# Optimization experiments

Hardware: AMD Instinct MI355X
Metric: run time of the kernel (lower is better)

The kernel has to match this reference:

```python
import jax, jax.numpy as jnp
import numpy as np

# --- Cl(5,0) geometric algebra with 32 basis blades (bitmask representation) ---
def _cayley():
    def sgn(a, b):
        # sign from reordering basis vectors (Euclidean metric: no metric signs)
        a >>= 1
        s = 0
        while a:
            s += bin(a & b).count('1')
            a >>= 1
        return -1.0 if (s & 1) else 1.0
    C = np.zeros((32, 32, 32), np.float32)
    for i in range(32):
        for j in range(32):
            C[i, j, i ^ j] = sgn(i, j)
    return jnp.asarray(C)

CAYLEY = _cayley()  # [32,32,32] structure constants
EPS = 1e-8

def geometric_product(a, b):
    # a, b: [..., 32]
    return jnp.einsum('...i,...j,ijk->...k', a, b, CAYLEY)

def manifold_normalization(x):
    # project multivector back to the unit-norm manifold
    return x * jax.lax.rsqrt(jnp.sum(x * x, axis=-1, keepdims=True) + EPS)


def setup_inputs() -> dict:
    key = jax.random.key(0)
    k1, k2, k3 = jax.random.split(key, 3)
    B, S, N, D = 16, 256, 16, 6
    H = 16  # hidden_channels
    x = jax.random.normal(k1, (B, S, N, D), dtype=jnp.float32)
    W_in = jax.random.normal(k2, (D, H * 32), dtype=jnp.float32) * 0.1
    b_in = jnp.zeros((H * 32,), dtype=jnp.float32)
    W_out = jax.random.normal(k3, (H * 32, D), dtype=jnp.float32) * 0.05
    b_out = jnp.zeros((D,), dtype=jnp.float32)
    return {"x": x, "W_in": W_in, "b_in": b_in, "W_out": W_out, "b_out": b_out}


def reference(x, W_in, b_in, W_out, b_out):
    B, S, N, D = x.shape
    H = W_in.shape[1] // 32
    # proj_in over the whole sequence at once
    x_embs = (x @ W_in + b_in).reshape(B, S, N, H, 32)
    # psi init: identity rotor (scalar blade = 1)
    psi0 = jnp.zeros((B, N, H, 32), dtype=x.dtype).at[..., 0].set(1.0)

    def step(psi, inp):
        u_t, x_t = inp  # [B,N,H,32], [B,N,D]
        delta_r = manifold_normalization(u_t.at[..., 0].add(1.0))
        psi = manifold_normalization(geometric_product(delta_r, psi))
        pred_delta = psi.reshape(B, N, H * 32) @ W_out + b_out
        return psi, x_t + pred_delta

    _, ys = jax.lax.scan(step, psi0,
                         (jnp.swapaxes(x_embs, 0, 1), jnp.swapaxes(x, 0, 1)))
    return jnp.swapaxes(ys, 0, 1)  # [B,S,N,D]
```

## Files before the change

### kernel.cpp

```cpp
#include <hip/hip_runtime.h>


#define EPS 1e-8f

constexpr int pcnt(int v) { int s = 0; while (v) { s += v & 1; v >>= 1; } return s; }
constexpr float sgnf(int a, int b) {
    a >>= 1; int s = 0;
    while (a) { s += pcnt(a & b); a >>= 1; }
    return (s & 1) ? -1.0f : 1.0f;
}
struct Tab16 {
    float sg2[16][16];
    float sig[16];
    int   cm[16];
};
constexpr Tab16 make16() {
    Tab16 t{};
    for (int c = 0; c < 16; ++c) {
        int m = c | ((pcnt(c) & 1) << 4);
        t.cm[c] = m;
        t.sig[c] = sgnf(m ^ 31, 31);
    }
    for (int i = 0; i < 16; ++i)
        for (int j = 0; j < 16; ++j)
            t.sg2[i][j] = sgnf(t.cm[i], t.cm[j]);
    return t;
}
__device__ constexpr Tab16 T16 = make16();

__global__ __launch_bounds__(256, 1) void k_prep(
        const float* __restrict__ W_in, const float* __restrict__ b_in,
        float* __restrict__ WP) {
    const int idx = blockIdx.x * 256 + threadIdx.x;
    if (idx >= 16 * 224) return;
    const int h = idx / 224, r = idx % 224;
    const int sg = r / 112, r2 = r % 112;
    const float pm = sg ? -1.0f : 1.0f;
    float val;
    if (r2 < 96) {
        const int d = r2 >> 4, c = r2 & 15, m = T16.cm[c];
        val = W_in[d * 512 + h * 32 + m]
            + pm * T16.sig[c] * W_in[d * 512 + h * 32 + (m ^ 31)];
    } else {
        const int c = r2 - 96, m = T16.cm[c];
        val = b_in[h * 32 + m] + pm * T16.sig[c] * b_in[h * 32 + (m ^ 31)];
    }
    WP[idx] = val;
}

__device__ __forceinline__ void build_u16(const float* __restrict__ Wsp,
                                          const float xv[6], float U[16]) {
#pragma unroll
    for (int c = 0; c < 16; ++c) U[c] = Wsp[96 + c];
#pragma unroll
    for (int d = 0; d < 6; ++d)
#pragma unroll
        for (int c = 0; c < 16; ++c)
            U[c] = fmaf(xv[d], Wsp[d * 16 + c], U[c]);
    U[0] += 1.0f;
}

__device__ __forceinline__ void gp16(float* __restrict__ np,
                                     const float* __restrict__ U,
                                     const float* __restrict__ R) {
#pragma unroll
    for (int c1 = 0; c1 < 16; ++c1)
#pragma unroll
        for (int c2 = 0; c2 < 16; ++c2)
            np[c1 ^ c2] = fmaf(T16.sg2[c1][c2] * U[c1], R[c2], np[c1 ^ c2]);
}

__device__ __forceinline__ float ssum32(const float* a, const float* b) {
    float s0 = 0.f, s1 = 0.f, s2 = 0.f, s3 = 0.f;
#pragma unroll
    for (int k = 0; k < 16; k += 4) {
        s0 = fmaf(a[k],     a[k],     s0); s1 = fmaf(a[k + 1], a[k + 1], s1);
        s2 = fmaf(a[k + 2], a[k + 2], s2); s3 = fmaf(a[k + 3], a[k + 3], s3);
        s0 = fmaf(b[k],     b[k],     s0); s1 = fmaf(b[k + 1], b[k + 1], s1);
        s2 = fmaf(b[k + 2], b[k + 2], s2); s3 = fmaf(b[k + 3], b[k + 3], s3);
    }
    return (s0 + s1) + (s2 + s3);
}

__global__ __launch_bounds__(256, 1) void k_fused(
        const float* __restrict__ x, const float* __restrict__ WP,
        const float* __restrict__ W_out, float* __restrict__ WS2) {
    const int lane = threadIdx.x & 63;
    const int wid = __builtin_amdgcn_readfirstlane(
        (int)(blockIdx.x * 4 + (threadIdx.x >> 6)));
    const int h = wid & 15, p = wid >> 4;
    const int sc = lane & 31;
    const int bn = p * 2 + (lane >> 5), b = bn >> 4, n = bn & 15;
    const float* __restrict__ Wp0 = WP + h * 224;
    const float* __restrict__ Wp1 = WP + h * 224 + 112;
    const float* __restrict__ Oh  = W_out + h * 192;

    float Ap[16], Am[16];
    {
        const int t = sc * 8;
        const float2* xp = (const float2*)(x + ((b * 256 + t) * 16 + n) * 6);
        float2 x01 = xp[0], x23 = xp[1], x45 = xp[2];
        const float xv[6] = {x01.x, x01.y, x23.x, x23.y, x45.x, x45.y};
        build_u16(Wp0, xv, Ap);
        build_u16(Wp1, xv, Am);
    }
    for (int i = 1; i < 8; ++i) {
        const int t = sc * 8 + i;
        const float2* xp = (const float2*)(x + ((b * 256 + t) * 16 + n) * 6);
        float2 x01 = xp[0], x23 = xp[1], x45 = xp[2];
        const float xv[6] = {x01.x, x01.y, x23.x, x23.y, x45.x, x45.y};
        float U[16], np[16];
        build_u16(Wp0, xv, U);
#pragma unroll
        for (int k = 0; k < 16; ++k) np[k] = 0.0f;
        gp16(np, U, Ap);
#pragma unroll
        for (int k = 0; k < 16; ++k) Ap[k] = np[k];
        build_u16(Wp1, xv, U);
#pragma unroll
        for (int k = 0; k < 16; ++k) np[k] = 0.0f;
        gp16(np, U, Am);
#pragma unroll
        for (int k = 0; k < 16; ++k) Am[k] = np[k];
    }
    {
        float rs = rsqrtf(0.5f * ssum32(Ap, Am) + EPS);
#pragma unroll
        for (int k = 0; k < 16; ++k) { Ap[k] *= rs; Am[k] *= rs; }
    }

#pragma unroll
    for (int k = 1; k < 32; k <<= 1) {
        float prp[16], prm[16];
#pragma unroll
        for (int j = 0; j < 16; ++j) {
            prp[j] = __shfl_up(Ap[j], k, 32);
            prm[j] = __shfl_up(Am[j], k, 32);
        }
        if (sc >= k) {
            float np[16];
#pragma unroll
            for (int m = 0; m < 16; ++m) np[m] = 0.0f;
            gp16(np, Ap, prp);
#pragma unroll
            for (int m = 0; m < 16; ++m) Ap[m] = np[m];
#pragma unroll
            for (int m = 0; m < 16; ++m) np[m] = 0.0f;
            gp16(np, Am, prm);
#pragma unroll
            for (int m = 0; m < 16; ++m) Am[m] = np[m];
        }
    }
    {
        float rs = rsqrtf(0.5f * ssum32(Ap, Am) + EPS);
#pragma unroll
        for (int j = 0; j < 16; ++j) { Ap[j] *= rs; Am[j] *= rs; }
    }
    float Rp[16], Rm[16];
#pragma unroll
    for (int j = 0; j < 16; ++j) {
        Rp[j] = __shfl_up(Ap[j], 1, 32);
        Rm[j] = __shfl_up(Am[j], 1, 32);
    }
    if (sc == 0) {
#pragma unroll
        for (int j = 0; j < 16; ++j) { Rp[j] = 0.0f; Rm[j] = 0.0f; }
        Rp[0] = 1.0f; Rm[0] = 1.0f;
    }

    for (int i = 0; i < 8; ++i) {
        const int t = sc * 8 + i;
        const float2* xp = (const float2*)(x + ((b * 256 + t) * 16 + n) * 6);
        float2 x01 = xp[0], x23 = xp[1], x45 = xp[2];
        const float xv[6] = {x01.x, x01.y, x23.x, x23.y, x45.x, x45.y};
        float U[16], npp[16], npm[16];
        build_u16(Wp0, xv, U);
#pragma unroll
        for (int k = 0; k < 16; ++k) npp[k] = 0.0f;
        gp16(npp, U, Rp);
        build_u16(Wp1, xv, U);
#pragma unroll
        for (int k = 0; k < 16; ++k) npm[k] = 0.0f;
        gp16(npm, U, Rm);
        float rs = 0.5f * rsqrtf(0.5f * ssum32(npp, npm) + EPS);
        float pd[6] = {0.f, 0.f, 0.f, 0.f, 0.f, 0.f};
#pragma unroll
        for (int c = 0; c < 16; ++c) {
            const int m = T16.cm[c];
            const float ev = npp[c] + npm[c];
            const float od = T16.sig[c] * (npp[c] - npm[c]);
#pragma unroll
            for (int d = 0; d < 6; ++d) {
                pd[d] = fmaf(ev, Oh[m * 6 + d], pd[d]);
                pd[d] = fmaf(od, Oh[(m ^ 31) * 6 + d], pd[d]);
            }
        }
#pragma unroll
        for (int k = 0; k < 16; ++k) { Rp[k] = npp[k]; Rm[k] = npm[k]; }
        float2* wp = (float2*)(WS2 + (((t * 16 + h) * 256) + bn) * 6);
        wp[0] = make_float2(pd[0] * rs, pd[1] * rs);
        wp[1] = make_float2(pd[2] * rs, pd[3] * rs);
        wp[2] = make_float2(pd[4] * rs, pd[5] * rs);
    }
}

__global__ __launch_bounds__(256, 1) void k_reduce(
        const float* __restrict__ x, const float* __restrict__ b_out,
        const float* __restrict__ WS2, float* __restrict__ out) {
    const int o = blockIdx.x * 256 + threadIdx.x;
    const int d = o % 6;
    const int r = o / 6;
    const int n = r & 15;
    const int r2 = r >> 4;
    const int t = r2 & 255;
    const int b = r2 >> 8;
    const int bn = b * 16 + n;
    float acc = x[o] + b_out[d];
#pragma unroll
    for (int h = 0; h < 16; ++h)
        acc += WS2[(((t * 16 + h) * 256) + bn) * 6 + d];
    out[o] = acc;
}

extern "C" void kernel_launch(void* const* d_in, const int* in_sizes, int n_in,
                              void* d_out, int out_size, void* d_ws, size_t ws_size,
                              hipStream_t stream) {
    (void)in_sizes; (void)n_in; (void)out_size; (void)ws_size;
    const float* x     = (const float*)d_in[0];
    const float* W_in  = (const float*)d_in[1];
    const float* b_in  = (const float*)d_in[2];
    const float* W_out = (const float*)d_in[3];
    const float* b_out = (const float*)d_in[4];
    float* out = (float*)d_out;

    float* WP  = (float*)d_ws;
    float* WS2 = (float*)((char*)d_ws + 16384);

    k_prep  <<<14,   256, 0, stream>>>(W_in, b_in, WP);
    k_fused <<<512,  256, 0, stream>>>(x, WP, W_out, WS2);
    k_reduce<<<1536, 256, 0, stream>>>(x, b_out, WS2, out);
}
```

Before: 144.7 us.

## Fuse head reduction into scan kernel via shared memory, widen scan to 64 lanes

Each block now handles one (b,n) pair with 16 waves (one per head), each wave scanning 256 timesteps with 64 lanes of 4 steps each instead of 32 lanes of 8. Per-head output contributions go to LDS, and after a barrier the block sums the 16 heads and writes the output directly. This removes the separate reduce kernel and the global workspace round trip. The cost is a longer parallel prefix scan (6 levels instead of 5), 96KB of LDS per block, and only 256 blocks of 1024 threads.

```diff
diff --git a/kernel.cpp b/kernel.cpp
--- a/kernel.cpp
+++ b/kernel.cpp
@@ -82,30 +82,32 @@
     return (s0 + s1) + (s2 + s3);
 }
 
-__global__ __launch_bounds__(256, 1) void k_fused(
+__global__ __launch_bounds__(1024, 1) void k_fused(
         const float* __restrict__ x, const float* __restrict__ WP,
-        const float* __restrict__ W_out, float* __restrict__ WS2) {
-    const int lane = threadIdx.x & 63;
-    const int wid = __builtin_amdgcn_readfirstlane(
-        (int)(blockIdx.x * 4 + (threadIdx.x >> 6)));
-    const int h = wid & 15, p = wid >> 4;
-    const int sc = lane & 31;
-    const int bn = p * 2 + (lane >> 5), b = bn >> 4, n = bn & 15;
+        const float* __restrict__ W_out, const float* __restrict__ b_out,
+        float* __restrict__ out) {
+    __shared__ float LP[16 * 1536];
+
+    const int tid  = threadIdx.x;
+    const int lane = tid & 63;
+    const int h = __builtin_amdgcn_readfirstlane((int)(tid >> 6));
+    const int bn = blockIdx.x, b = bn >> 4, n = bn & 15;
+    const int sc = lane;
     const float* __restrict__ Wp0 = WP + h * 224;
     const float* __restrict__ Wp1 = WP + h * 224 + 112;
     const float* __restrict__ Oh  = W_out + h * 192;
 
     float Ap[16], Am[16];
     {
-        const int t = sc * 8;
+        const int t = sc * 4;
         const float2* xp = (const float2*)(x + ((b * 256 + t) * 16 + n) * 6);
         float2 x01 = xp[0], x23 = xp[1], x45 = xp[2];
         const float xv[6] = {x01.x, x01.y, x23.x, x23.y, x45.x, x45.y};
         build_u16(Wp0, xv, Ap);
         build_u16(Wp1, xv, Am);
     }
-    for (int i = 1; i < 8; ++i) {
-        const int t = sc * 8 + i;
+    for (int i = 1; i < 4; ++i) {
+        const int t = sc * 4 + i;
         const float2* xp = (const float2*)(x + ((b * 256 + t) * 16 + n) * 6);
         float2 x01 = xp[0], x23 = xp[1], x45 = xp[2];
         const float xv[6] = {x01.x, x01.y, x23.x, x23.y, x45.x, x45.y};
@@ -130,12 +132,12 @@
     }
 
 #pragma unroll
-    for (int k = 1; k < 32; k <<= 1) {
+    for (int k = 1; k < 64; k <<= 1) {
         float prp[16], prm[16];
 #pragma unroll
         for (int j = 0; j < 16; ++j) {
-            prp[j] = __shfl_up(Ap[j], k, 32);
-            prm[j] = __shfl_up(Am[j], k, 32);
+            prp[j] = __shfl_up(Ap[j], k, 64);
+            prm[j] = __shfl_up(Am[j], k, 64);
         }
         if (sc >= k) {
             float np[16];
@@ -159,8 +161,8 @@
     float Rp[16], Rm[16];
 #pragma unroll
     for (int j = 0; j < 16; ++j) {
-        Rp[j] = __shfl_up(Ap[j], 1, 32);
-        Rm[j] = __shfl_up(Am[j], 1, 32);
+        Rp[j] = __shfl_up(Ap[j], 1, 64);
+        Rm[j] = __shfl_up(Am[j], 1, 64);
     }
     if (sc == 0) {
 #pragma unroll
@@ -168,8 +170,8 @@
         Rp[0] = 1.0f; Rm[0] = 1.0f;
     }
 
-    for (int i = 0; i < 8; ++i) {
-        const int t = sc * 8 + i;
+    for (int i = 0; i < 4; ++i) {
+        const int t = sc * 4 + i;
         const float2* xp = (const float2*)(x + ((b * 256 + t) * 16 + n) * 6);
         float2 x01 = xp[0], x23 = xp[1], x45 = xp[2];
         const float xv[6] = {x01.x, x01.y, x23.x, x23.y, x45.x, x45.y};
@@ -197,29 +199,21 @@
         }
 #pragma unroll
         for (int k = 0; k < 16; ++k) { Rp[k] = npp[k]; Rm[k] = npm[k]; }
-        float2* wp = (float2*)(WS2 + (((t * 16 + h) * 256) + bn) * 6);
-        wp[0] = make_float2(pd[0] * rs, pd[1] * rs);
-        wp[1] = make_float2(pd[2] * rs, pd[3] * rs);
-        wp[2] = make_float2(pd[4] * rs, pd[5] * rs);
-    }
-}
-
-__global__ __launch_bounds__(256, 1) void k_reduce(
-        const float* __restrict__ x, const float* __restrict__ b_out,
-        const float* __restrict__ WS2, float* __restrict__ out) {
-    const int o = blockIdx.x * 256 + threadIdx.x;
-    const int d = o % 6;
-    const int r = o / 6;
-    const int n = r & 15;
-    const int r2 = r >> 4;
-    const int t = r2 & 255;
-    const int b = r2 >> 8;
-    const int bn = b * 16 + n;
-    float acc = x[o] + b_out[d];
-#pragma unroll
-    for (int h = 0; h < 16; ++h)
-        acc += WS2[(((t * 16 + h) * 256) + bn) * 6 + d];
-    out[o] = acc;
+        float2* lp = (float2*)(LP + h * 1536 + t * 6);
+        lp[0] = make_float2(pd[0] * rs, pd[1] * rs);
+        lp[1] = make_float2(pd[2] * rs, pd[3] * rs);
+        lp[2] = make_float2(pd[4] * rs, pd[5] * rs);
+    }
+
+    __syncthreads();
+
+    for (int slot = tid; slot < 1536; slot += 1024) {
+        const int t = slot / 6, d = slot - t * 6;
+        float acc = x[((b * 256 + t) * 16 + n) * 6 + d] + b_out[d];
+#pragma unroll
+        for (int hh = 0; hh < 16; ++hh) acc += LP[hh * 1536 + slot];
+        out[((b * 256 + t) * 16 + n) * 6 + d] = acc;
+    }
 }
 
 extern "C" void kernel_launch(void* const* d_in, const int* in_sizes, int n_in,
@@ -233,10 +227,8 @@
     const float* b_out = (const float*)d_in[4];
     float* out = (float*)d_out;
 
-    float* WP  = (float*)d_ws;
-    float* WS2 = (float*)((char*)d_ws + 16384);
-
-    k_prep  <<<14,   256, 0, stream>>>(W_in, b_in, WP);
-    k_fused <<<512,  256, 0, stream>>>(x, WP, W_out, WS2);
-    k_reduce<<<1536, 256, 0, stream>>>(x, b_out, WS2, out);
-}
+    float* WP = (float*)d_ws;
+
+    k_prep <<<14,  256,  0, stream>>>(W_in, b_in, WP);
+    k_fused<<<256, 1024, 0, stream>>>(x, WP, W_out, b_out, out);
+}
```

Result: slower. 212.2 us (+46.6%).

## Pre-reduce four hidden channels per block in shared memory before global write

Applied to the files above, without the earlier changes.

Each block now holds the four warps for the same (b,n) pair and hidden group, so per-timestep outputs are staged in LDS and summed across the four heads before going to global. This divides the workspace written by the fused kernel, and read by the reduce kernel, by four. The global layout is reordered so the reduce kernel reads contiguously per block. In exchange it adds 48KB of shared memory, a block barrier and a remapping of block indices.

```diff
diff --git a/kernel.cpp b/kernel.cpp
--- a/kernel.cpp
+++ b/kernel.cpp
@@ -84,12 +84,16 @@
 
 __global__ __launch_bounds__(256, 1) void k_fused(
         const float* __restrict__ x, const float* __restrict__ WP,
-        const float* __restrict__ W_out, float* __restrict__ WS2) {
-    const int lane = threadIdx.x & 63;
-    const int wid = __builtin_amdgcn_readfirstlane(
-        (int)(blockIdx.x * 4 + (threadIdx.x >> 6)));
-    const int h = wid & 15, p = wid >> 4;
-    const int sc = lane & 31;
+        const float* __restrict__ W_out, float* __restrict__ WS4) {
+    __shared__ float LP[4 * 8 * 64 * 6];
+
+    const int tid  = threadIdx.x;
+    const int lane = tid & 63;
+    const int w    = __builtin_amdgcn_readfirstlane((int)(tid >> 6));
+    const int hg   = blockIdx.x & 3;
+    const int p    = blockIdx.x >> 2;
+    const int h    = 4 * hg + w;
+    const int sc   = lane & 31;
     const int bn = p * 2 + (lane >> 5), b = bn >> 4, n = bn & 15;
     const float* __restrict__ Wp0 = WP + h * 224;
     const float* __restrict__ Wp1 = WP + h * 224 + 112;
@@ -197,28 +201,37 @@
         }
 #pragma unroll
         for (int k = 0; k < 16; ++k) { Rp[k] = npp[k]; Rm[k] = npm[k]; }
-        float2* wp = (float2*)(WS2 + (((t * 16 + h) * 256) + bn) * 6);
-        wp[0] = make_float2(pd[0] * rs, pd[1] * rs);
-        wp[1] = make_float2(pd[2] * rs, pd[3] * rs);
-        wp[2] = make_float2(pd[4] * rs, pd[5] * rs);
+        float* lp = LP + ((w * 8 + i) * 64 + lane) * 6;
+#pragma unroll
+        for (int d = 0; d < 6; ++d) lp[d] = pd[d] * rs;
+    }
+
+    __syncthreads();
+
+    float* outp = WS4 + (hg * 128 + p) * 3072;
+    for (int s = tid; s < 3072; s += 256) {
+        const int d = s % 6, tc = s / 6;
+        const int c = tc & 1, t = tc >> 1;
+        const int li = ((t & 7) * 64 + (c * 32 + (t >> 3))) * 6 + d;
+        float acc = LP[0 * 3072 + li] + LP[1 * 3072 + li]
+                  + LP[2 * 3072 + li] + LP[3 * 3072 + li];
+        outp[s] = acc;
     }
 }
 
 __global__ __launch_bounds__(256, 1) void k_reduce(
         const float* __restrict__ x, const float* __restrict__ b_out,
-        const float* __restrict__ WS2, float* __restrict__ out) {
-    const int o = blockIdx.x * 256 + threadIdx.x;
-    const int d = o % 6;
-    const int r = o / 6;
-    const int n = r & 15;
-    const int r2 = r >> 4;
-    const int t = r2 & 255;
-    const int b = r2 >> 8;
-    const int bn = b * 16 + n;
+        const float* __restrict__ WS4, float* __restrict__ out) {
+    const int idx = blockIdx.x * 256 + threadIdx.x;
+    const int p = idx / 3072, s = idx % 3072;
+    const int d = s % 6, tc = s / 6;
+    const int c = tc & 1, t = tc >> 1;
+    const int bn = p * 2 + c, b = bn >> 4, n = bn & 15;
+    const int o = ((b * 256 + t) * 16 + n) * 6 + d;
     float acc = x[o] + b_out[d];
 #pragma unroll
-    for (int h = 0; h < 16; ++h)
-        acc += WS2[(((t * 16 + h) * 256) + bn) * 6 + d];
+    for (int hg = 0; hg < 4; ++hg)
+        acc += WS4[(hg * 128 + p) * 3072 + s];
     out[o] = acc;
 }
 
@@ -234,9 +247,9 @@
     float* out = (float*)d_out;
 
     float* WP  = (float*)d_ws;
-    float* WS2 = (float*)((char*)d_ws + 16384);
+    float* WS4 = (float*)((char*)d_ws + 16384);
 
     k_prep  <<<14,   256, 0, stream>>>(W_in, b_in, WP);
-    k_fused <<<512,  256, 0, stream>>>(x, WP, W_out, WS2);
-    k_reduce<<<1536, 256, 0, stream>>>(x, b_out, WS2, out);
-}
+    k_fused <<<512,  256, 0, stream>>>(x, WP, W_out, WS4);
+    k_reduce<<<1536, 256, 0, stream>>>(x, b_out, WS4, out);
+}
```

Result: faster. 134.7 us (-6.9%).
